# Optimization experiments

Measured on AMD Instinct MI355X. Metric: run time of the kernel, lower is better.

Reference implementation:

```python
import jax, jax.numpy as jnp
import numpy as np

D_MODEL, D_QKV, N_HEADS = 1024, 64, 16


def setup_inputs() -> dict:
    key = jax.random.key(0)
    k_x, k_qkv, k_out = jax.random.split(key, 3)
    X = jax.random.normal(k_x, (2, 2048, D_MODEL), dtype=jnp.float32)
    # nn.Linear(d_model, 3*d_qkv*n_heads, bias=False): store as (in, out) for X @ W
    W_qkv = jax.random.normal(k_qkv, (D_MODEL, 3 * D_QKV * N_HEADS), dtype=jnp.float32) * (D_MODEL ** -0.5)
    W_out = jax.random.normal(k_out, (D_QKV * N_HEADS, D_MODEL), dtype=jnp.float32) * ((D_QKV * N_HEADS) ** -0.5)
    return {"X": X, "W_qkv": W_qkv, "W_out": W_out}


def reference(X, W_qkv, W_out):
    b, s, _ = X.shape
    h, d = N_HEADS, D_QKV
    scale = d ** 0.5
    qkv = X @ W_qkv                          # [b, s, 3*h*d]
    # Faithful to torch: view(b, s, h, d, 3).unbind(-1) -> interleaved q/k/v layout
    qkv = qkv.reshape(b, s, h, d, 3)
    q, k, v = qkv[..., 0], qkv[..., 1], qkv[..., 2]   # each [b, s, h, d]
    scores = jnp.einsum("bqhd,bkhd->bhqk", q, k) / scale
    weights = jax.nn.softmax(scores, axis=-1)          # [b, h, s, s]
    attn = jnp.einsum("bhqk,bkhd->bqhd", weights, v)   # [b, s, h, d]
    return attn.reshape(b, s, h * d) @ W_out           # [b, s, d_model]
```

## Files before the change

kernel.cpp:

```cpp
#include <hip/hip_runtime.h>
#include <hip/hip_bf16.h>
#include <math.h>

typedef __bf16 bf16;
typedef __bf16 bf16x2 __attribute__((ext_vector_type(2)));
typedef __bf16 bf16x4 __attribute__((ext_vector_type(4)));
typedef __bf16 bf16x8 __attribute__((ext_vector_type(8)));
typedef float f32x4 __attribute__((ext_vector_type(4)));
typedef float f32x16 __attribute__((ext_vector_type(16)));
typedef int i32x2 __attribute__((ext_vector_type(2)));
typedef int i32x4 __attribute__((ext_vector_type(4)));

#define MFMA16(a, b, c) __builtin_amdgcn_mfma_f32_16x16x32_bf16(a, b, c, 0, 0, 0)
#define MFMA32(a, b, c) __builtin_amdgcn_mfma_f32_32x32x16_bf16(a, b, c, 0, 0, 0)

constexpr int D_MODEL = 1024;
constexpr int N_QKV   = 3072;
constexpr int BATCH   = 2;
constexpr int SEQ     = 2048;
constexpr int NH      = 16;
constexpr int DH      = 64;
constexpr int M_TOT   = BATCH * SEQ;

__device__ __forceinline__ void gl_lds16(const bf16* g, bf16* l) {
    __builtin_amdgcn_global_load_lds(
        (const __attribute__((address_space(1))) void*)g,
        (__attribute__((address_space(3))) void*)l, 16, 0, 0);
}

__device__ __forceinline__ void pl32swap(int& a, int& b) {
    i32x2 r = __builtin_amdgcn_permlane32_swap(a, b, false, false);
    a = r[0];
    b = r[1];
}

__device__ __forceinline__ void transpose_tile(
    const float* __restrict__ in, bf16* __restrict__ out,
    int K, int N, int n0, int k0, bf16 (*T)[72], bool permute)
{
    const int tid = threadIdx.x;
    const int r   = tid >> 2;
    const int c4  = (tid & 3) * 16;

    const float* src = in + (size_t)(k0 + r) * N + n0 + c4;
    f32x4 v0 = *(const f32x4*)(src + 0);
    f32x4 v1 = *(const f32x4*)(src + 4);
    f32x4 v2 = *(const f32x4*)(src + 8);
    f32x4 v3 = *(const f32x4*)(src + 12);
    #pragma unroll
    for (int j = 0; j < 4; j++) {
        T[c4 + j][r]      = (bf16)v0[j];
        T[c4 + 4 + j][r]  = (bf16)v1[j];
        T[c4 + 8 + j][r]  = (bf16)v2[j];
        T[c4 + 12 + j][r] = (bf16)v3[j];
    }
    __syncthreads();
    int rowg = n0 + r;
    if (permute) {
        const int which = rowg % 3;
        const int h     = rowg / 192;
        const int d     = (rowg % 192) / 3;
        rowg = which * 1024 + h * 64 + d;
    }
    bf16* dst = out + (size_t)rowg * K + k0 + c4;
    *(bf16x8*)(dst)     = *(const bf16x8*)&T[r][c4];
    *(bf16x8*)(dst + 8) = *(const bf16x8*)&T[r][c4 + 8];
}

__global__ __launch_bounds__(256) void prepass_kernel(
    const float* __restrict__ X, const float* __restrict__ Wqkv,
    const float* __restrict__ Wout,
    bf16* __restrict__ xb, bf16* __restrict__ wqkv_t, bf16* __restrict__ wout_t)
{
    __shared__ bf16 T[64][72];
    const int b = blockIdx.x;
    if (b < 2048) {
        const size_t i = ((size_t)b * 256 + threadIdx.x) * 8;
        f32x4 a0 = *(const f32x4*)(X + i);
        f32x4 a1 = *(const f32x4*)(X + i + 4);
        bf16x8 w;
        #pragma unroll
        for (int j = 0; j < 4; j++) { w[j] = (bf16)a0[j]; w[j + 4] = (bf16)a1[j]; }
        *(bf16x8*)(xb + i) = w;
    } else if (b < 2048 + 768) {
        const int idx = b - 2048;
        transpose_tile(Wqkv, wqkv_t, D_MODEL, N_QKV,
                       (idx % 48) * 64, (idx / 48) * 64, T, true);
    } else {
        const int idx = b - 2816;
        transpose_tile(Wout, wout_t, D_MODEL, D_MODEL,
                       (idx % 16) * 64, (idx / 16) * 64, T, false);
    }
}

__global__ __launch_bounds__(256) void qkv_gemm_kernel(
    const bf16* __restrict__ Xb, const bf16* __restrict__ Wt,
    bf16* __restrict__ qb, bf16* __restrict__ kb, bf16* __restrict__ vb)
{
    __shared__ __align__(16) bf16 smem[2 * 128 * 64];
    bf16* As = smem;
    bf16* Bs = smem + 128 * 64;

    const int tid  = threadIdx.x;
    const int wave = tid >> 6;
    const int lane = tid & 63;
    const int quad = lane >> 4;
    const int l16  = lane & 15;
    const int sw   = l16 & 7;
    const int m0   = blockIdx.x * 128;
    const int n0   = blockIdx.y * 128;
    const int wm   = (wave & 1) * 64;
    const int wn   = (wave >> 1) * 64;

    const int srow = lane >> 3;
    const int sc_s = ((lane & 7) ^ srow) * 8;
    const int sc_d = (lane & 7) * 8;

    f32x4 acc[4][4];
    #pragma unroll
    for (int a = 0; a < 4; a++)
        #pragma unroll
        for (int b = 0; b < 4; b++) acc[a][b] = {0.f, 0.f, 0.f, 0.f};

    for (int kb0 = 0; kb0 < D_MODEL; kb0 += 64) {
        __syncthreads();
        #pragma unroll
        for (int j = 0; j < 4; j++) {
            const int row = wave * 32 + j * 8 + srow;
            gl_lds16(Xb + (size_t)(m0 + row) * D_MODEL + kb0 + sc_s,
                     As + row * 64 + sc_d);
            gl_lds16(Wt + (size_t)(n0 + row) * D_MODEL + kb0 + sc_s,
                     Bs + row * 64 + sc_d);
        }
        __syncthreads();

        #pragma unroll
        for (int ks = 0; ks < 2; ks++) {
            const int co = ((ks * 4 + quad) ^ sw) * 8;
            bf16x8 af[4], bfr[4];
            #pragma unroll
            for (int mi = 0; mi < 4; mi++)
                af[mi] = *(const bf16x8*)&As[(wm + mi * 16 + l16) * 64 + co];
            #pragma unroll
            for (int ni = 0; ni < 4; ni++)
                bfr[ni] = *(const bf16x8*)&Bs[(wn + ni * 16 + l16) * 64 + co];
            #pragma unroll
            for (int mi = 0; mi < 4; mi++)
                #pragma unroll
                for (int ni = 0; ni < 4; ni++)
                    acc[mi][ni] = MFMA16(af[mi], bfr[ni], acc[mi][ni]);
        }
    }

    const int bb = m0 >> 11;
    if (n0 < 2048) {
        bf16* dst0 = (n0 < 1024) ? qb : kb;
        #pragma unroll
        for (int ni = 0; ni < 4; ni++) {
            const int n = n0 + wn + ni * 16 + l16;
            const int h = (n >> 6) & 15;
            const int d = n & 63;
            #pragma unroll
            for (int mi = 0; mi < 4; mi++) {
                const int s0 = (m0 + wm + mi * 16 + quad * 4) & (SEQ - 1);
                const size_t bh = (size_t)(bb * NH + h);
                #pragma unroll
                for (int i = 0; i < 4; i++)
                    dst0[(bh * SEQ + s0 + i) * DH + d] = (bf16)acc[mi][ni][i];
            }
        }
    } else {
        __syncthreads();
        bf16* T = smem;
        #pragma unroll
        for (int ni = 0; ni < 4; ni++) {
            const int nl = wn + ni * 16 + l16;
            #pragma unroll
            for (int mi = 0; mi < 4; mi++) {
                const int ml = wm + mi * 16 + quad * 4;
                bf16x4 pv;
                #pragma unroll
                for (int i = 0; i < 4; i++) pv[i] = (bf16)acc[mi][ni][i];
                const int c   = ml >> 3;
                const int swz = (c & 8) | ((c ^ nl) & 7);
                *(bf16x4*)&T[nl * 128 + swz * 8 + (ml & 7)] = pv;
            }
        }
        __syncthreads();
        const int hbase  = (n0 - 2048) >> 6;
        const int s_base = m0 & (SEQ - 1);
        #pragma unroll
        for (int it = 0; it < 8; it++) {
            const int nl = (tid >> 4) + it * 16;
            const int mc = tid & 15;
            const int swz = (mc & 8) | ((mc ^ nl) & 7);
            bf16x8 vv = *(const bf16x8*)&T[nl * 128 + swz * 8];
            const int h = hbase + (nl >> 6);
            const int d = nl & 63;
            *(bf16x8*)(vb + ((size_t)(bb * NH + h) * DH + d) * SEQ
                       + s_base + mc * 8) = vv;
        }
    }
}

__global__ __launch_bounds__(512, 4) void attn_kernel(
    const bf16* __restrict__ qb, const bf16* __restrict__ kb,
    const bf16* __restrict__ vb, bf16* __restrict__ ob)
{
    __shared__ __align__(16) bf16 smem[32768];

    const int tid  = threadIdx.x;
    const int wave = tid >> 6;
    const int grp  = wave >> 2;
    const int wq   = wave & 3;
    const int lane = tid & 63;
    const int l32  = lane & 31;
    const int hi   = lane >> 5;
    const int ltid = tid & 255;
    const int bh   = blockIdx.x;
    const int q0   = blockIdx.y * 128;
    const size_t base  = (size_t)bh * SEQ * DH;
    const int    kbase = grp * (SEQ / 2);

    bf16* const KsB = smem + grp * 2 * 4096;
    bf16* const VtB = smem + 16384 + grp * 2 * 4096;

    constexpr float QSCALE = 0.125f * 1.44269504f;

    bf16x8 qf[4];
    {
        const size_t qoff = base + (size_t)(q0 + wq * 32 + l32) * DH + hi * 8;
        #pragma unroll
        for (int kc = 0; kc < 4; kc++) {
            qf[kc] = *(const bf16x8*)(qb + qoff + kc * 16);
            #pragma unroll
            for (int j = 0; j < 8; j++)
                qf[kc][j] = (bf16)((float)qf[kc][j] * QSCALE);
        }
    }

    f32x16 o_acc[2];
    #pragma unroll
    for (int i = 0; i < 16; i++) { o_acc[0][i] = 0.f; o_acc[1][i] = 0.f; }
    float l_acc = 0.f;

    const int so0 = ltid;
    const int so1 = 256 + ltid;
    const int sr0 = so0 >> 3, sc0 = ((so0 & 7) ^ (sr0 & 7)) * 8;
    const int sr1 = so1 >> 3, sc1 = ((so1 & 7) ^ (sr1 & 7)) * 8;

    #define STAGE(bufi, kk0)                                                   \
        do {                                                                   \
            gl_lds16(kb + base + (size_t)(kbase + (kk0) + sr0) * DH + sc0,     \
                     KsB + (bufi) * 4096 + so0 * 8);                           \
            gl_lds16(kb + base + (size_t)(kbase + (kk0) + sr1) * DH + sc1,     \
                     KsB + (bufi) * 4096 + so1 * 8);                           \
            gl_lds16(vb + base + (size_t)sr0 * SEQ + kbase + (kk0) + sc0,      \
                     VtB + (bufi) * 4096 + so0 * 8);                           \
            gl_lds16(vb + base + (size_t)sr1 * SEQ + kbase + (kk0) + sc1,      \
                     VtB + (bufi) * 4096 + so1 * 8);                           \
        } while (0)

    STAGE(0, 0);
    int buf = 0;

    for (int kt = 0; kt < SEQ / 128; ++kt) {
        __syncthreads();
        if (kt + 1 < SEQ / 128) STAGE(buf ^ 1, (kt + 1) * 64);

        const bf16* Kst = KsB + buf * 4096;
        const bf16* Vtt = VtB + buf * 4096;

        #pragma unroll
        for (int kblk = 0; kblk < 2; kblk++) {
            f32x16 sacc;
            #pragma unroll
            for (int i = 0; i < 16; i++) sacc[i] = 0.f;
            #pragma unroll
            for (int kc = 0; kc < 4; kc++) {
                const int cko = ((2 * kc + hi) ^ (l32 & 7)) * 8;
                bf16x8 kf = *(const bf16x8*)
                    &Kst[(kblk * 32 + l32) * 64 + cko];
                sacc = MFMA32(kf, qf[kc], sacc);
            }

            int w[8];
            #pragma unroll
            for (int c = 0; c < 8; c++) {
                const float e0 = __builtin_amdgcn_exp2f(sacc[2 * c]);
                const float e1 = __builtin_amdgcn_exp2f(sacc[2 * c + 1]);
                l_acc += e0;
                l_acc += e1;
                bf16x2 t; t[0] = (bf16)e0; t[1] = (bf16)e1;
                w[c] = __builtin_bit_cast(int, t);
            }
            #pragma unroll
            for (int cc = 0; cc < 2; cc++) {
                pl32swap(w[cc * 4 + 0], w[cc * 4 + 2]);
                pl32swap(w[cc * 4 + 1], w[cc * 4 + 3]);
                i32x4 fi = {w[cc * 4 + 0], w[cc * 4 + 1],
                            w[cc * 4 + 2], w[cc * 4 + 3]};
                bf16x8 pa = __builtin_bit_cast(bf16x8, fi);

                const int kc = kblk * 2 + cc;
                const int cko = ((2 * kc + hi) ^ (l32 & 7)) * 8;
                #pragma unroll
                for (int nb = 0; nb < 2; nb++) {
                    bf16x8 vf = *(const bf16x8*)
                        &Vtt[(nb * 32 + l32) * 64 + cko];
                    o_acc[nb] = MFMA32(pa, vf, o_acc[nb]);
                }
            }
        }
        buf ^= 1;
    }
    #undef STAGE

    const float l_q = l_acc + __shfl_xor(l_acc, 32);

    float* cO  = (float*)smem;
    float* cL1 = (float*)smem + 8192;
    float* cL2 = (float*)smem + 8320;

    __syncthreads();
    if (grp == 1) {
        #pragma unroll
        for (int nb = 0; nb < 2; nb++)
            #pragma unroll
            for (int c4 = 0; c4 < 4; c4++) {
                const int j = nb * 4 + c4;
                f32x4 v = { o_acc[nb][c4 * 4 + 0], o_acc[nb][c4 * 4 + 1],
                            o_acc[nb][c4 * 4 + 2], o_acc[nb][c4 * 4 + 3] };
                *(f32x4*)&cO[(wq * 64 + lane) * 32 + ((j ^ (lane & 7)) * 4)] = v;
            }
        if (hi == 0) cL1[wq * 32 + l32] = l_q;
    }
    __syncthreads();
    if (grp == 0) {
        #pragma unroll
        for (int nb = 0; nb < 2; nb++)
            #pragma unroll
            for (int c4 = 0; c4 < 4; c4++) {
                const int j = nb * 4 + c4;
                f32x4 v = *(const f32x4*)
                    &cO[(wq * 64 + lane) * 32 + ((j ^ (lane & 7)) * 4)];
                #pragma unroll
                for (int e = 0; e < 4; e++) o_acc[nb][c4 * 4 + e] += v[e];
            }
        if (hi == 0) cL2[wq * 32 + l32] = l_q + cL1[wq * 32 + l32];
    }
    __syncthreads();
    if (grp == 0) {
        const int b = bh >> 4, h = bh & 15;
        #pragma unroll
        for (int i = 0; i < 16; i++) {
            const int qrow = (i & 3) + 8 * (i >> 2) + 4 * hi;
            const int q = q0 + wq * 32 + qrow;
            const float li = 1.0f / cL2[wq * 32 + qrow];
            #pragma unroll
            for (int nb = 0; nb < 2; nb++)
                ob[((size_t)(b * SEQ + q) * NH + h) * DH + nb * 32 + l32] =
                    (bf16)(o_acc[nb][i] * li);
        }
    }
}

__global__ __launch_bounds__(256) void out_gemm_kernel(
    const bf16* __restrict__ A, const bf16* __restrict__ Wt,
    float* __restrict__ out)
{
    __shared__ __align__(16) bf16 As[128 * 64];
    __shared__ __align__(16) bf16 Bs[128 * 64];

    const int tid  = threadIdx.x;
    const int wave = tid >> 6;
    const int lane = tid & 63;
    const int quad = lane >> 4;
    const int l16  = lane & 15;
    const int sw   = l16 & 7;
    const int m0   = blockIdx.x * 128;
    const int n0   = blockIdx.y * 128;
    const int wm   = (wave & 1) * 64;
    const int wn   = (wave >> 1) * 64;

    const int srow = lane >> 3;
    const int sc_s = ((lane & 7) ^ srow) * 8;
    const int sc_d = (lane & 7) * 8;

    f32x4 acc[4][4];
    #pragma unroll
    for (int a = 0; a < 4; a++)
        #pragma unroll
        for (int b = 0; b < 4; b++) acc[a][b] = {0.f, 0.f, 0.f, 0.f};

    for (int kb0 = 0; kb0 < D_MODEL; kb0 += 64) {
        __syncthreads();
        #pragma unroll
        for (int j = 0; j < 4; j++) {
            const int row = wave * 32 + j * 8 + srow;
            gl_lds16(A  + (size_t)(m0 + row) * D_MODEL + kb0 + sc_s,
                     As + row * 64 + sc_d);
            gl_lds16(Wt + (size_t)(n0 + row) * D_MODEL + kb0 + sc_s,
                     Bs + row * 64 + sc_d);
        }
        __syncthreads();

        #pragma unroll
        for (int ks = 0; ks < 2; ks++) {
            const int co = ((ks * 4 + quad) ^ sw) * 8;
            bf16x8 af[4], bfr[4];
            #pragma unroll
            for (int mi = 0; mi < 4; mi++)
                af[mi] = *(const bf16x8*)&As[(wm + mi * 16 + l16) * 64 + co];
            #pragma unroll
            for (int ni = 0; ni < 4; ni++)
                bfr[ni] = *(const bf16x8*)&Bs[(wn + ni * 16 + l16) * 64 + co];
            #pragma unroll
            for (int mi = 0; mi < 4; mi++)
                #pragma unroll
                for (int ni = 0; ni < 4; ni++)
                    acc[mi][ni] = MFMA16(af[mi], bfr[ni], acc[mi][ni]);
        }
    }

    #pragma unroll
    for (int mi = 0; mi < 4; mi++) {
        const int row0 = m0 + wm + mi * 16 + quad * 4;
        #pragma unroll
        for (int ni = 0; ni < 4; ni++) {
            const int n = n0 + wn + ni * 16 + l16;
            #pragma unroll
            for (int i = 0; i < 4; i++)
                out[(size_t)(row0 + i) * D_MODEL + n] = acc[mi][ni][i];
        }
    }
}

extern "C" void kernel_launch(void* const* d_in, const int* in_sizes, int n_in,
                              void* d_out, int out_size, void* d_ws, size_t ws_size,
                              hipStream_t stream)
{
    const float* X    = (const float*)d_in[0];
    const float* Wqkv = (const float*)d_in[1];
    const float* Wout = (const float*)d_in[2];
    float* out        = (float*)d_out;

    const size_t n_elem = (size_t)M_TOT * D_MODEL;
    bf16* qb      = (bf16*)d_ws;
    bf16* kb      = qb + n_elem;
    bf16* vb      = kb + n_elem;
    bf16* attnb   = vb + n_elem;
    bf16* wqkv_t  = attnb + n_elem;
    bf16* wout_t  = wqkv_t + (size_t)N_QKV * D_MODEL;
    bf16* xb      = wout_t + (size_t)D_MODEL * D_MODEL;

    prepass_kernel<<<3072, 256, 0, stream>>>(X, Wqkv, Wout, xb, wqkv_t, wout_t);

    qkv_gemm_kernel<<<dim3(M_TOT / 128, N_QKV / 128), 256, 0, stream>>>(
        xb, wqkv_t, qb, kb, vb);
    attn_kernel<<<dim3(BATCH * NH, SEQ / 128), 512, 0, stream>>>(qb, kb, vb, attnb);
    out_gemm_kernel<<<dim3(M_TOT / 128, D_MODEL / 128), 256, 0, stream>>>(
        attnb, wout_t, out);
}
```

Before: 183.9 us.

## Rewrite QKV GEMM with 256x256 tiles and 4-stage async LDS pipeline

The QKV projection GEMM moves from 128x128 tiles with 256 threads and a single-buffered load/sync loop to 256x256 tiles with 512 threads. It uses a 4-stage ring of global-to-LDS loads with explicit vmcnt waits, raw barriers and s_setprio around the MFMA block. The aim is to hide global load latency behind MFMA work and raise data reuse per tile. The cost is 128KB of LDS and much higher register pressure, and the grid shrinks to 192 blocks, which may leave some of the 256 CUs idle.

```diff
diff --git a/kernel.cpp b/kernel.cpp
--- a/kernel.cpp
+++ b/kernel.cpp
@@ -32,6 +32,13 @@
     i32x2 r = __builtin_amdgcn_permlane32_swap(a, b, false, false);
     a = r[0];
     b = r[1];
+}
+
+template <int N> __device__ __forceinline__ void waitv() {
+    asm volatile("s_waitcnt vmcnt(%0)" :: "n"(N) : "memory");
+}
+__device__ __forceinline__ void waitlgkm0() {
+    asm volatile("s_waitcnt lgkmcnt(0)" ::: "memory");
 }
 
 __device__ __forceinline__ void transpose_tile(
@@ -93,77 +100,102 @@
     }
 }
 
-__global__ __launch_bounds__(256) void qkv_gemm_kernel(
+__global__ __launch_bounds__(512, 2) void qkv_gemm_kernel(
     const bf16* __restrict__ Xb, const bf16* __restrict__ Wt,
     bf16* __restrict__ qb, bf16* __restrict__ kb, bf16* __restrict__ vb)
 {
-    __shared__ __align__(16) bf16 smem[2 * 128 * 64];
-    bf16* As = smem;
-    bf16* Bs = smem + 128 * 64;
+    __shared__ __align__(16) bf16 smem[65536];
+    bf16* const sA = smem;
+    bf16* const sB = smem + 32768;
 
     const int tid  = threadIdx.x;
     const int wave = tid >> 6;
     const int lane = tid & 63;
     const int quad = lane >> 4;
     const int l16  = lane & 15;
-    const int sw   = l16 & 7;
-    const int m0   = blockIdx.x * 128;
-    const int n0   = blockIdx.y * 128;
-    const int wm   = (wave & 1) * 64;
-    const int wn   = (wave >> 1) * 64;
-
-    const int srow = lane >> 3;
-    const int sc_s = ((lane & 7) ^ srow) * 8;
-    const int sc_d = (lane & 7) * 8;
-
-    f32x4 acc[4][4];
+    const int wr   = wave >> 2;
+    const int wc   = wave & 3;
+    const int m0   = blockIdx.x * 256;
+    const int n0   = blockIdx.y * 256;
+
+    const int sr2  = tid >> 3;
+    const int c8p  = (tid & 7) ^ (sr2 & 7);
+    const int stR0 = (sr2 << 1) | (c8p >> 2);
+    const int stC0 = (c8p & 3) << 3;
+
+    const bf16* Asrc = Xb + (size_t)(m0 + stR0) * D_MODEL + stC0;
+    const bf16* Bsrc = Wt + (size_t)(n0 + stR0) * D_MODEL + stC0;
+
+#define STG(s, kbo)                                                          \
+    do {                                                                     \
+        gl_lds16(Asrc + (kbo),                 sA + (s) * 8192 + tid * 8);   \
+        gl_lds16(Asrc + 128 * D_MODEL + (kbo), sA + (s) * 8192 + 4096 + tid * 8); \
+        gl_lds16(Bsrc + (kbo),                 sB + (s) * 8192 + tid * 8);   \
+        gl_lds16(Bsrc + 128 * D_MODEL + (kbo), sB + (s) * 8192 + 4096 + tid * 8); \
+    } while (0)
+
+    const int foff = ((l16 >> 1) << 6) +
+                     (((((l16 & 1) << 2) | quad) ^ ((l16 >> 1) & 7)) << 3);
+
+    f32x4 acc[8][4];
     #pragma unroll
-    for (int a = 0; a < 4; a++)
+    for (int a = 0; a < 8; a++)
         #pragma unroll
         for (int b = 0; b < 4; b++) acc[a][b] = {0.f, 0.f, 0.f, 0.f};
 
-    for (int kb0 = 0; kb0 < D_MODEL; kb0 += 64) {
-        __syncthreads();
-        #pragma unroll
-        for (int j = 0; j < 4; j++) {
-            const int row = wave * 32 + j * 8 + srow;
-            gl_lds16(Xb + (size_t)(m0 + row) * D_MODEL + kb0 + sc_s,
-                     As + row * 64 + sc_d);
-            gl_lds16(Wt + (size_t)(n0 + row) * D_MODEL + kb0 + sc_s,
-                     Bs + row * 64 + sc_d);
-        }
-        __syncthreads();
-
-        #pragma unroll
-        for (int ks = 0; ks < 2; ks++) {
-            const int co = ((ks * 4 + quad) ^ sw) * 8;
-            bf16x8 af[4], bfr[4];
-            #pragma unroll
-            for (int mi = 0; mi < 4; mi++)
-                af[mi] = *(const bf16x8*)&As[(wm + mi * 16 + l16) * 64 + co];
-            #pragma unroll
-            for (int ni = 0; ni < 4; ni++)
-                bfr[ni] = *(const bf16x8*)&Bs[(wn + ni * 16 + l16) * 64 + co];
-            #pragma unroll
-            for (int mi = 0; mi < 4; mi++)
-                #pragma unroll
-                for (int ni = 0; ni < 4; ni++)
-                    acc[mi][ni] = MFMA16(af[mi], bfr[ni], acc[mi][ni]);
-        }
-    }
-
-    const int bb = m0 >> 11;
+#define PHASE(s, jn, DOSTG, WV)                                              \
+    {                                                                        \
+        const bf16* Ab_ = sA + (s) * 8192 + wr * 4096;                       \
+        const bf16* Bb_ = sB + (s) * 8192 + wc * 2048;                       \
+        bf16x8 af[8], bfr[4];                                                \
+        _Pragma("unroll") for (int mi = 0; mi < 8; mi++)                     \
+            af[mi] = *(const bf16x8*)&Ab_[mi * 512 + foff];                  \
+        _Pragma("unroll") for (int ni = 0; ni < 4; ni++)                     \
+            bfr[ni] = *(const bf16x8*)&Bb_[ni * 512 + foff];                 \
+        waitlgkm0();                                                         \
+        __builtin_amdgcn_s_barrier();                                        \
+        if (DOSTG) { STG((s), (jn) * 32); }                                  \
+        __builtin_amdgcn_s_setprio(1);                                       \
+        _Pragma("unroll") for (int mi = 0; mi < 8; mi++)                     \
+            _Pragma("unroll") for (int ni = 0; ni < 4; ni++)                 \
+                acc[mi][ni] = MFMA16(af[mi], bfr[ni], acc[mi][ni]);          \
+        __builtin_amdgcn_s_setprio(0);                                       \
+        waitv<WV>();                                                         \
+        __builtin_amdgcn_s_barrier();                                        \
+    }
+
+    STG(0, 0); STG(1, 32); STG(2, 64); STG(3, 96);
+    waitv<12>();
+    __builtin_amdgcn_s_barrier();
+
+    for (int t = 0; t < 7; ++t) {
+        const int j = t * 4;
+        PHASE(0, j + 4, true, 12)
+        PHASE(1, j + 5, true, 12)
+        PHASE(2, j + 6, true, 12)
+        PHASE(3, j + 7, true, 12)
+    }
+    PHASE(0, 0, false, 8)
+    PHASE(1, 0, false, 4)
+    PHASE(2, 0, false, 0)
+    PHASE(3, 0, false, 0)
+
+#undef PHASE
+#undef STG
+
+    const int bb     = m0 >> 11;
+    const int s_base = m0 & (SEQ - 1);
+
     if (n0 < 2048) {
         bf16* dst0 = (n0 < 1024) ? qb : kb;
-        #pragma unroll
-        for (int ni = 0; ni < 4; ni++) {
-            const int n = n0 + wn + ni * 16 + l16;
-            const int h = (n >> 6) & 15;
-            const int d = n & 63;
-            #pragma unroll
-            for (int mi = 0; mi < 4; mi++) {
-                const int s0 = (m0 + wm + mi * 16 + quad * 4) & (SEQ - 1);
-                const size_t bh = (size_t)(bb * NH + h);
+        const int h = ((n0 + wc * 64) >> 6) & 15;
+        const size_t bh = (size_t)(bb * NH + h);
+        #pragma unroll
+        for (int mi = 0; mi < 8; mi++) {
+            const int s0 = s_base + wr * 128 + mi * 16 + quad * 4;
+            #pragma unroll
+            for (int ni = 0; ni < 4; ni++) {
+                const int d = ni * 16 + l16;
                 #pragma unroll
                 for (int i = 0; i < 4; i++)
                     dst0[(bh * SEQ + s0 + i) * DH + d] = (bf16)acc[mi][ni][i];
@@ -174,31 +206,33 @@
         bf16* T = smem;
         #pragma unroll
         for (int ni = 0; ni < 4; ni++) {
-            const int nl = wn + ni * 16 + l16;
-            #pragma unroll
-            for (int mi = 0; mi < 4; mi++) {
-                const int ml = wm + mi * 16 + quad * 4;
+            const int nl = wc * 64 + ni * 16 + l16;
+            #pragma unroll
+            for (int mi = 0; mi < 8; mi++) {
+                const int ml = wr * 128 + mi * 16 + quad * 4;
                 bf16x4 pv;
                 #pragma unroll
                 for (int i = 0; i < 4; i++) pv[i] = (bf16)acc[mi][ni][i];
                 const int c   = ml >> 3;
-                const int swz = (c & 8) | ((c ^ nl) & 7);
-                *(bf16x4*)&T[nl * 128 + swz * 8 + (ml & 7)] = pv;
+                const int swz = (c & 24) | ((c ^ nl) & 7);
+                *(bf16x4*)&T[nl * 256 + swz * 8 + (ml & 7)] = pv;
             }
         }
         __syncthreads();
-        const int hbase  = (n0 - 2048) >> 6;
-        const int s_base = m0 & (SEQ - 1);
+        const int hbase = (n0 - 2048) >> 6;
         #pragma unroll
         for (int it = 0; it < 8; it++) {
-            const int nl = (tid >> 4) + it * 16;
-            const int mc = tid & 15;
-            const int swz = (mc & 8) | ((mc ^ nl) & 7);
-            bf16x8 vv = *(const bf16x8*)&T[nl * 128 + swz * 8];
-            const int h = hbase + (nl >> 6);
-            const int d = nl & 63;
-            *(bf16x8*)(vb + ((size_t)(bb * NH + h) * DH + d) * SEQ
-                       + s_base + mc * 8) = vv;
+            const int nl = (tid >> 4) + it * 32;
+            const int h  = hbase + (nl >> 6);
+            const int d  = nl & 63;
+            const size_t obase = ((size_t)(bb * NH + h) * DH + d) * SEQ + s_base;
+            #pragma unroll
+            for (int cc = 0; cc < 2; cc++) {
+                const int c   = (tid & 15) + cc * 16;
+                const int swz = (c & 24) | ((c ^ nl) & 7);
+                bf16x8 vv = *(const bf16x8*)&T[nl * 256 + swz * 8];
+                *(bf16x8*)(vb + obase + c * 8) = vv;
+            }
         }
     }
 }
@@ -456,7 +490,7 @@
 
     prepass_kernel<<<3072, 256, 0, stream>>>(X, Wqkv, Wout, xb, wqkv_t, wout_t);
 
-    qkv_gemm_kernel<<<dim3(M_TOT / 128, N_QKV / 128), 256, 0, stream>>>(
+    qkv_gemm_kernel<<<dim3(M_TOT / 256, N_QKV / 256), 512, 0, stream>>>(
         xb, wqkv_t, qb, kb, vb);
     attn_kernel<<<dim3(BATCH * NH, SEQ / 128), 512, 0, stream>>>(qb, kb, vb, attnb);
     out_gemm_kernel<<<dim3(M_TOT / 128, D_MODEL / 128), 256, 0, stream>>>(
```

Result: faster. 176.7 us (-3.9%).
